# Kernel tuning notes

Measured on AMD Instinct MI355X. Metric: run time of the kernel, lower is better.

Reference implementation:

```python
import jax, jax.numpy as jnp
import numpy as np

N_STEPS = 5
STATE_DIM = 512
ANN_DIM = 256
N_NODES = 2048
N_EDGE_TYPES = 4


def setup_inputs() -> dict:
    key = jax.random.key(0)
    ks = jax.random.split(key, 12)
    D, E, N = STATE_DIM, N_EDGE_TYPES, N_NODES
    s = 0.02
    adjacency = (jax.random.uniform(ks[0], (N, N * 2 * E)) < 0.015).astype(jnp.float32)
    annotations = jax.random.normal(ks[1], (N, ANN_DIM), dtype=jnp.float32)
    W_prop = jax.random.normal(ks[2], (2 * E, D, D), dtype=jnp.float32) * s
    b_prop = jnp.zeros((2 * E, D), dtype=jnp.float32)
    Wz = jax.random.normal(ks[3], (D, D), dtype=jnp.float32) * s
    Uz = jax.random.normal(ks[4], (D, D), dtype=jnp.float32) * s
    bz = jnp.zeros((D,), dtype=jnp.float32)
    Wr = jax.random.normal(ks[5], (D, D), dtype=jnp.float32) * s
    Ur = jax.random.normal(ks[6], (D, D), dtype=jnp.float32) * s
    br = jnp.zeros((D,), dtype=jnp.float32)
    Wh = jax.random.normal(ks[7], (D, D), dtype=jnp.float32) * s
    Uh = jax.random.normal(ks[8], (D, D), dtype=jnp.float32) * s
    bh = jnp.zeros((D,), dtype=jnp.float32)
    return dict(adjacency=adjacency, annotations=annotations, W_prop=W_prop, b_prop=b_prop,
                Wz=Wz, Uz=Uz, bz=bz, Wr=Wr, Ur=Ur, br=br, Wh=Wh, Uh=Uh, bh=bh)


def reference(adjacency, annotations, W_prop, b_prop, Wz, Uz, bz, Wr, Ur, br, Wh, Uh, bh):
    N = annotations.shape[0]
    D = W_prop.shape[-1]
    # pad annotations into first columns of state (input1[:, :ann_dim] = annotations)
    h = jnp.zeros((N, D), dtype=annotations.dtype).at[:, :annotations.shape[1]].set(annotations)
    for _ in range(N_STEPS):
        # per-edge-type linear transforms: edge_type_list [2E, N, D]
        t = jnp.einsum('nd,edf->enf', h, W_prop) + b_prop[:, None, :]
        # adjacency aggregation: A is [N, N*2E] with per-edge-type column blocks
        a = adjacency @ t.reshape(-1, D)  # [N, D]
        # GRU node update (UpdateNet)
        z = jax.nn.sigmoid(a @ Wz + h @ Uz + bz)
        r = jax.nn.sigmoid(a @ Wr + h @ Ur + br)
        h_tilde = jnp.tanh(a @ Wh + (r * h) @ Uh + bh)
        h = (1.0 - z) * h + z * h_tilde
    return h
```

## Files before the change

kernel.cpp:

```cpp
#include <hip/hip_runtime.h>

typedef __attribute__((ext_vector_type(8))) short short8;
typedef __attribute__((ext_vector_type(4))) float floatx4;
typedef __attribute__((ext_vector_type(2))) unsigned uintx2;

#define NSTEPS 5
#define DD 512
#define ANN 256
#define NNODE 2048
#define NEDGE 8
#define NCOLS (NNODE * NEDGE)
#define MAXE 96
#define KP (NEDGE * DD)
#define NND (NNODE * DD)


typedef __attribute__((address_space(3))) unsigned lds_u32;
typedef const __attribute__((address_space(1))) unsigned g_u32;
__device__ __forceinline__ void gload16(const short* g, short* l) {
    __builtin_amdgcn_global_load_lds((g_u32*)g, (lds_u32*)l, 16, 0, 0);
}

__device__ inline float bf2f(unsigned short s) {
    unsigned u = ((unsigned)s) << 16;
    float f; __builtin_memcpy(&f, &u, 4);
    return f;
}
__device__ inline unsigned short f2bf(float f) {
    unsigned u; __builtin_memcpy(&u, &f, 4);
    u += 0x7fffu + ((u >> 16) & 1u);
    return (unsigned short)(u >> 16);
}
__device__ inline void split2(float x, unsigned short& hi, unsigned short& lo) {
    hi = f2bf(x);
    lo = f2bf(x - bf2f(hi));
}
__device__ inline void fo_write(short* __restrict__ Fhi, short* __restrict__ Flo,
                                int row, int col, float v) {
    unsigned short hs, ls;
    split2(v, hs, ls);
    size_t a = ((size_t)(row >> 4) * 64 + (col >> 3)) * 128 + ((row & 15) << 3) + (col & 7);
    Fhi[a] = (short)hs;
    Flo[a] = (short)ls;
}
__device__ inline void fo_write2(short* __restrict__ Fhi, short* __restrict__ Flo,
                                 int row, int c, float v0, float v1) {
    unsigned short h0, l0, h1, l1;
    split2(v0, h0, l0);
    split2(v1, h1, l1);
    size_t a = ((size_t)(row >> 4) * 64 + (c >> 3)) * 128 + ((row & 15) << 3) + (c & 7);
    *(unsigned*)(Fhi + a) = (unsigned)h0 | ((unsigned)h1 << 16);
    *(unsigned*)(Flo + a) = (unsigned)l0 | ((unsigned)l1 << 16);
}

__global__ __launch_bounds__(256) void k_init(const float* __restrict__ ann,
                                              float* __restrict__ h,
                                              short* __restrict__ HBhi,
                                              short* __restrict__ HBlo,
                                              int* __restrict__ cnt2,
                                              unsigned short* __restrict__ idx) {
    int n = blockIdx.x, t = threadIdx.x;
    int c = 2 * t;
    float v0 = 0.f, v1 = 0.f;
    if (c < ANN) {
        v0 = ann[(size_t)n * ANN + c];
        v1 = ann[(size_t)n * ANN + c + 1];
    }
    h[(size_t)n * DD + c]     = v0;
    h[(size_t)n * DD + c + 1] = v1;
    fo_write2(HBhi, HBlo, n, c, v0, v1);
    if (t < NEDGE) cnt2[n * NEDGE + t] = 0;
    unsigned* ip = (unsigned*)(idx + (size_t)n * NEDGE * MAXE);
    for (int j = t; j < NEDGE * MAXE / 2; j += 256)
        ip[j] = 2048u | (2048u << 16);
    if (n == 0) {
        h[(size_t)NNODE * DD + c]     = 0.f;
        h[(size_t)NNODE * DD + c + 1] = 0.f;
    }
}

__global__ __launch_bounds__(256) void k_build(const float* __restrict__ adj,
                                               int* __restrict__ cnt2,
                                               unsigned short* __restrict__ idx) {
    int n = blockIdx.x;
    const float* row = adj + (size_t)n * NCOLS;
    for (int j8 = threadIdx.x; j8 < NCOLS / 8; j8 += 256) {
        floatx4 a = *(const floatx4*)(row + j8 * 8);
        floatx4 b = *(const floatx4*)(row + j8 * 8 + 4);
        unsigned nz = 0;
        #pragma unroll
        for (int i = 0; i < 4; i++) {
            if (a[i] != 0.f) nz |= 1u << i;
            if (b[i] != 0.f) nz |= 1u << (4 + i);
        }
        while (nz) {
            int i = __builtin_ctz(nz);
            nz &= nz - 1;
            int j = j8 * 8 + i;
            int e = j >> 11;
            int m = j & (NNODE - 1);
            int p = atomicAdd(&cnt2[n * NEDGE + e], 1);
            if (p < MAXE) idx[((size_t)n * NEDGE + e) * MAXE + p] = (unsigned short)m;
        }
    }
}

__global__ __launch_bounds__(256) void k_transP(const float* __restrict__ W,
                                                short* __restrict__ Fhi,
                                                short* __restrict__ Flo, int K) {
    __shared__ float st[32][33];
    int tx = threadIdx.x & 31, ty = threadIdx.x >> 5;
    int k0 = blockIdx.x * 32, n0 = blockIdx.y * 32;
    #pragma unroll
    for (int i = 0; i < 4; i++)
        st[ty + i * 8][tx] = W[(size_t)(k0 + ty + i * 8) * DD + n0 + tx];
    __syncthreads();
    #pragma unroll
    for (int i = 0; i < 4; i++) {
        int n = n0 + ty + i * 8, k = k0 + tx;
        float v = st[tx][ty + i * 8];
        unsigned short hs, ls;
        split2(v, hs, ls);
        size_t a = ((size_t)(n >> 4) * (K >> 3) + (k >> 3)) * 128 + ((n & 15) << 3) + (k & 7);
        Fhi[a] = (short)hs;
        Flo[a] = (short)ls;
    }
}

__global__ __launch_bounds__(256) void k_transG(const float* __restrict__ s00,
                                                const float* __restrict__ s10,
                                                const float* __restrict__ s01,
                                                const float* __restrict__ s11,
                                                short* __restrict__ Fhi,
                                                short* __restrict__ Flo) {
    __shared__ float st[32][33];
    const int K = 2 * DD;
    int tx = threadIdx.x & 31, ty = threadIdx.x >> 5;
    int k0 = blockIdx.x * 32, n0 = blockIdx.y * 32;
    const float* sk0 = (n0 < DD) ? s00 : s01;
    const float* sk1 = (n0 < DD) ? s10 : s11;
    #pragma unroll
    for (int i = 0; i < 4; i++) {
        int k = k0 + ty + i * 8;
        const float* s = (k < DD) ? sk0 : sk1;
        st[ty + i * 8][tx] = s[(size_t)(k & (DD - 1)) * DD + ((n0 + tx) & (DD - 1))];
    }
    __syncthreads();
    #pragma unroll
    for (int i = 0; i < 4; i++) {
        int n = n0 + ty + i * 8, k = k0 + tx;
        float v = st[tx][ty + i * 8];
        unsigned short hs, ls;
        split2(v, hs, ls);
        size_t a = ((size_t)(n >> 4) * (K >> 3) + (k >> 3)) * 128 + ((n & 15) << 3) + (k & 7);
        Fhi[a] = (short)hs;
        Flo[a] = (short)ls;
    }
}

__global__ __launch_bounds__(256) void k_gather_all(const float* __restrict__ h,
                                                    const int* __restrict__ cnt2,
                                                    const unsigned short* __restrict__ idx,
                                                    short* __restrict__ Gbhi,
                                                    short* __restrict__ Gblo) {
    __shared__ unsigned short sidx[8 * MAXE];
    __shared__ int scnt[8];
    const int bid = blockIdx.x;
    const int ep = bid & 3;
    const int g  = bid >> 2;
    const int n0 = g * 4;
    const int t  = threadIdx.x;
    const int dn = t >> 6;
    const int th2 = t & 63;

    if (t < 8) scnt[t] = cnt2[(n0 + (t >> 1)) * NEDGE + 2 * ep + (t & 1)];
    {
        const unsigned* src0 = (const unsigned*)(idx + ((size_t)n0 * NEDGE + 2 * ep) * MAXE);
        for (int j = t; j < 384; j += 256) {
            int d = j / 96;
            int w = j - d * 96;
            ((unsigned*)sidx)[d * 96 + w] = src0[(size_t)d * (NEDGE * MAXE / 2) + w];
        }
    }
    __syncthreads();

    const float* hp = h + 8 * th2;

    floatx4 e0c0, e0c1, e1c0, e1c1;
    auto gather_edge = [&](int le, floatx4& o0, floatx4& o1) {
        int m = scnt[dn * 2 + le];
        m = m > MAXE ? MAXE : m;
        m = (m + 3) & ~3;
        const unsigned short* row = &sidx[dn * 192 + le * 96];
        floatx4 a0 = (floatx4){0.f, 0.f, 0.f, 0.f};
        floatx4 a1 = (floatx4){0.f, 0.f, 0.f, 0.f};
        floatx4 b0 = (floatx4){0.f, 0.f, 0.f, 0.f};
        floatx4 b1 = (floatx4){0.f, 0.f, 0.f, 0.f};
        for (int i = 0; i < m; i += 4) {
            uintx2 w = *(const uintx2*)(row + i);
            const float* r0 = hp + (size_t)(w[0] & 0xffffu) * DD;
            const float* r1 = hp + (size_t)(w[0] >> 16) * DD;
            const float* r2 = hp + (size_t)(w[1] & 0xffffu) * DD;
            const float* r3 = hp + (size_t)(w[1] >> 16) * DD;
            floatx4 v0 = *(const floatx4*)r0;
            floatx4 v1 = *(const floatx4*)(r0 + 4);
            floatx4 v2 = *(const floatx4*)r1;
            floatx4 v3 = *(const floatx4*)(r1 + 4);
            floatx4 v4 = *(const floatx4*)r2;
            floatx4 v5 = *(const floatx4*)(r2 + 4);
            floatx4 v6 = *(const floatx4*)r3;
            floatx4 v7 = *(const floatx4*)(r3 + 4);
            a0 += v0; a1 += v1; b0 += v2; b1 += v3;
            a0 += v4; a1 += v5; b0 += v6; b1 += v7;
        }
        o0 = a0 + b0;
        o1 = a1 + b1;
    };
    gather_edge(0, e0c0, e0c1);
    gather_edge(1, e1c0, e1c1);

    __syncthreads();

    #pragma unroll
    for (int le = 0; le < 2; le++) {
        floatx4 c0 = le ? e1c0 : e0c0;
        floatx4 c1 = le ? e1c1 : e0c1;
        int ge = 2 * ep + le;
        unsigned short hs[8], ls[8];
        #pragma unroll
        for (int j = 0; j < 4; j++) {
            split2(c0[j], hs[j], ls[j]);
            split2(c1[j], hs[4 + j], ls[4 + j]);
        }
        short8 hv, lv;
        #pragma unroll
        for (int j = 0; j < 8; j++) { hv[j] = (short)hs[j]; lv[j] = (short)ls[j]; }
        size_t a = ((size_t)(n0 >> 4) * 512 + ge * 64 + th2) * 128
                 + (size_t)((n0 & 15) + dn) * 8;
        *(short8*)(Gbhi + a) = hv;
        *(short8*)(Gblo + a) = lv;
    }
}

template<int MODE>
__global__ __launch_bounds__(256, 4) void k_gemm8(
    const short* __restrict__ A0hi, const short* __restrict__ A0lo,
    const short* __restrict__ A1hi, const short* __restrict__ A1lo,
    const short* __restrict__ Bhi,  const short* __restrict__ Blo,
    const float* __restrict__ bias0, const float* __restrict__ bias1,
    float* __restrict__ zbuf,
    float* __restrict__ h,
    short* __restrict__ Ohi, short* __restrict__ Olo,
    float* __restrict__ Pb) {

    __shared__ short S[24][512];

    const int tid = threadIdx.x;
    const int lane = tid & 63;
    const int wave = tid >> 6;
    const int wm = wave >> 1;
    const int wn = wave & 1;
    const int quad = lane >> 4;
    const int l16 = lane & 15;

    const int pbid = blockIdx.x;
    const int x = pbid & 7;
    const int j = pbid >> 3;
    const int mband = x * 4 + (j & 3);
    int kh, bx;
    if (MODE == 1) { kh = 0; bx = j >> 2; }
    else           { kh = (j >> 2) & 1; bx = j >> 3; }
    const int blockM = mband * 64;
    const int blockN = bx * 32;
    const int mt0 = blockM >> 4, nt0 = blockN >> 4;
    const int KCB = (MODE == 0) ? 512 : 128;
    const int bko = (MODE == 0) ? kh * 256 : (MODE == 2 ? kh * 64 : 0);
    const int Kloc = (MODE == 0) ? 2048 : (MODE == 1 ? 1024 : 512);

    const short* Ahi_s = (MODE == 2 && kh) ? A1hi : A0hi;
    const short* Alo_s = (MODE == 2 && kh) ? A1lo : A0lo;

    floatx4 acc[2];
    acc[0] = (floatx4){0.f, 0.f, 0.f, 0.f};
    acc[1] = (floatx4){0.f, 0.f, 0.f, 0.f};

    auto gaddr = [&](int k0, int s) -> const short* {
        if (s < 16) {
            int pl = s >> 3, u = s & 7;
            int mt = u >> 1, ks = u & 1;
            const short* base;
            int kc, stride;
            if (MODE == 0) {
                base = pl ? A0lo : A0hi;
                kc = kh * 256 + (k0 >> 3) + ks * 4;
                stride = 512;
            } else if (MODE == 1) {
                int seg = k0 >> 9;
                base = seg ? (pl ? A1lo : A1hi) : (pl ? A0lo : A0hi);
                kc = ((k0 & 511) >> 3) + ks * 4;
                stride = 64;
            } else {
                base = pl ? Alo_s : Ahi_s;
                kc = (k0 >> 3) + ks * 4;
                stride = 64;
            }
            return base + ((size_t)(mt0 + mt) * stride + kc) * 128;
        } else {
            int u = s - 16, pl = u >> 2, ks = (u >> 1) & 1, nt = u & 1;
            const short* base = pl ? Blo : Bhi;
            return base + ((size_t)(nt0 + nt) * KCB + bko + (k0 >> 3) + ks * 4) * 128;
        }
    };

    const short* gp[6];
    short* lp[6];
    #pragma unroll
    for (int jj = 0; jj < 6; jj++) {
        int s = jj * 4 + wave;
        gp[jj] = gaddr(0, s) + lane * 8;
        lp[jj] = &S[s][lane * 8];
    }

    const int SEGK = (MODE == 1) ? 512 : Kloc;
    #pragma unroll 1
    for (int seg = 0; seg < Kloc / SEGK; seg++) {
        if (MODE == 1 && seg == 1) {
            #pragma unroll
            for (int jj = 0; jj < 6; jj++) {
                int s = jj * 4 + wave;
                gp[jj] = gaddr(512, s) + lane * 8;
            }
        }
        #pragma unroll 1
        for (int k0 = 0; k0 < SEGK; k0 += 64) {
            #pragma unroll
            for (int jj = 0; jj < 6; jj++) {
                gload16(gp[jj], lp[jj]);
                gp[jj] += 1024;
            }
            __syncthreads();

            #pragma unroll
            for (int ks = 0; ks < 2; ks++) {
                short8 ah[2], al[2], bh, bl;
                #pragma unroll
                for (int mi = 0; mi < 2; mi++) {
                    ah[mi] = *(const short8*)&S[(wm * 2 + mi) * 2 + ks][lane * 8];
                    al[mi] = *(const short8*)&S[8 + (wm * 2 + mi) * 2 + ks][lane * 8];
                }
                bh = *(const short8*)&S[16 + ks * 2 + wn][lane * 8];
                bl = *(const short8*)&S[20 + ks * 2 + wn][lane * 8];
                #pragma unroll
                for (int mi = 0; mi < 2; mi++) {
                    acc[mi] = __builtin_amdgcn_mfma_f32_16x16x32_bf16(ah[mi], bh, acc[mi], 0, 0, 0);
                    acc[mi] = __builtin_amdgcn_mfma_f32_16x16x32_bf16(ah[mi], bl, acc[mi], 0, 0, 0);
                    acc[mi] = __builtin_amdgcn_mfma_f32_16x16x32_bf16(al[mi], bh, acc[mi], 0, 0, 0);
                }
            }
            __syncthreads();
        }
    }

    float* P = Pb + (size_t)kh * NND;
    #pragma unroll
    for (int mi = 0; mi < 2; mi++) {
        int gcol = blockN + wn * 16 + l16;
        #pragma unroll
        for (int r = 0; r < 4; r++) {
            int grow = blockM + wm * 32 + mi * 16 + quad * 4 + r;
            float v = acc[mi][r];
            if (MODE == 0 || MODE == 2) {
                P[(size_t)grow * DD + gcol] = v;
            } else {
                if (gcol < DD) {
                    size_t o = (size_t)grow * DD + gcol;
                    zbuf[o] = 1.f / (1.f + __expf(-(v + bias0[gcol])));
                } else {
                    int c = gcol - DD;
                    size_t o = (size_t)grow * DD + c;
                    float rr = 1.f / (1.f + __expf(-(v + bias1[c])));
                    fo_write(Ohi, Olo, grow, c, rr * h[o]);
                }
            }
        }
    }
}

__global__ __launch_bounds__(256) void k_combP(const float* __restrict__ Pb,
                                               const int* __restrict__ cnt2,
                                               const float* __restrict__ bp,
                                               short* __restrict__ Gahi,
                                               short* __restrict__ Galo) {
    int n = blockIdx.x, t = threadIdx.x;
    int c = 2 * t;
    float s0 = 0.f, s1 = 0.f;
    #pragma unroll
    for (int e = 0; e < NEDGE; e++) {
        float ce = (float)cnt2[n * NEDGE + e];
        s0 += ce * bp[e * DD + c];
        s1 += ce * bp[e * DD + c + 1];
    }
    size_t o = (size_t)n * DD + c;
    float v0 = Pb[o] + Pb[o + NND] + s0;
    float v1 = Pb[o + 1] + Pb[o + 1 + NND] + s1;
    fo_write2(Gahi, Galo, n, c, v0, v1);
}

__global__ __launch_bounds__(256) void k_combF(const float* __restrict__ Pb,
                                               const float* __restrict__ bh,
                                               const float* __restrict__ zbuf,
                                               float* __restrict__ h,
                                               short* __restrict__ HBhi,
                                               short* __restrict__ HBlo,
                                               float* __restrict__ outF) {
    int n = blockIdx.x, t = threadIdx.x;
    int c = 2 * t;
    size_t o = (size_t)n * DD + c;
    float hn0, hn1;
    {
        float v = Pb[o] + Pb[o + NND] + bh[c];
        hn0 = (1.f - zbuf[o]) * h[o] + zbuf[o] * tanhf(v);
    }
    {
        float v = Pb[o + 1] + Pb[o + 1 + NND] + bh[c + 1];
        hn1 = (1.f - zbuf[o + 1]) * h[o + 1] + zbuf[o + 1] * tanhf(v);
    }
    h[o] = hn0;
    h[o + 1] = hn1;
    fo_write2(HBhi, HBlo, n, c, hn0, hn1);
    outF[o] = hn0;
    outF[o + 1] = hn1;
}

extern "C" void kernel_launch(void* const* d_in, const int* in_sizes, int n_in,
                              void* d_out, int out_size, void* d_ws, size_t ws_size,
                              hipStream_t stream) {
    const float* adj = (const float*)d_in[0];
    const float* ann = (const float*)d_in[1];
    const float* Wp  = (const float*)d_in[2];
    const float* bp  = (const float*)d_in[3];
    const float* Wz  = (const float*)d_in[4];
    const float* Uz  = (const float*)d_in[5];
    const float* bz  = (const float*)d_in[6];
    const float* Wr  = (const float*)d_in[7];
    const float* Ur  = (const float*)d_in[8];
    const float* br  = (const float*)d_in[9];
    const float* Wh  = (const float*)d_in[10];
    const float* Uh  = (const float*)d_in[11];
    const float* bh  = (const float*)d_in[12];

    char* p = (char*)d_ws;
    float* h     = (float*)p; p += (size_t)(NNODE + 1) * DD * 4;
    float* abuf  = (float*)p; p += (size_t)NNODE * DD * 4;
    float* Pb    = (float*)p; p += (size_t)4 * NND * 4;
    short* Gbhi  = (short*)p; p += (size_t)NNODE * KP * 2;
    short* Gblo  = (short*)p; p += (size_t)NNODE * KP * 2;
    short* Gahi  = (short*)p; p += (size_t)NNODE * DD * 2;
    short* Galo  = (short*)p; p += (size_t)NNODE * DD * 2;
    short* HBhi  = (short*)p; p += (size_t)NNODE * DD * 2;
    short* HBlo  = (short*)p; p += (size_t)NNODE * DD * 2;
    short* RHhi  = (short*)p; p += (size_t)NNODE * DD * 2;
    short* RHlo  = (short*)p; p += (size_t)NNODE * DD * 2;
    short* WpThi = (short*)p; p += (size_t)DD * KP * 2;
    short* WpTlo = (short*)p; p += (size_t)DD * KP * 2;
    short* ZRhi  = (short*)p; p += (size_t)(2 * DD) * (2 * DD) * 2;
    short* ZRlo  = (short*)p; p += (size_t)(2 * DD) * (2 * DD) * 2;
    short* HThi  = (short*)p; p += (size_t)DD * (2 * DD) * 2;
    short* HTlo  = (short*)p; p += (size_t)DD * (2 * DD) * 2;
    unsigned short* idx = (unsigned short*)p;
    p += (size_t)NNODE * NEDGE * MAXE * 2;
    int* cnt2 = (int*)p; p += (size_t)NNODE * NEDGE * 4;

    float* outF = (float*)d_out;

    k_init<<<NNODE, 256, 0, stream>>>(ann, h, HBhi, HBlo, cnt2, idx);
    k_build<<<NNODE, 256, 0, stream>>>(adj, cnt2, idx);
    k_transP<<<dim3(KP / 32, DD / 32), 256, 0, stream>>>(Wp, WpThi, WpTlo, KP);
    k_transG<<<dim3(32, 32), 256, 0, stream>>>(Wz, Uz, Wr, Ur, ZRhi, ZRlo);
    k_transG<<<dim3(32, 16), 256, 0, stream>>>(Wh, Uh, Wh, Uh, HThi, HTlo);

    for (int s = 0; s < NSTEPS; s++) {
        k_gather_all<<<2048, 256, 0, stream>>>(h, cnt2, idx, Gbhi, Gblo);
        k_gemm8<0><<<1024, 256, 0, stream>>>(Gbhi, Gblo, nullptr, nullptr,
                                             WpThi, WpTlo, nullptr, nullptr,
                                             nullptr, nullptr, nullptr, nullptr, Pb);
        k_combP<<<NNODE, 256, 0, stream>>>(Pb, cnt2, bp, Gahi, Galo);
        k_gemm8<1><<<1024, 256, 0, stream>>>(Gahi, Galo, HBhi, HBlo,
                                             ZRhi, ZRlo, bz, br,
                                             abuf, h, RHhi, RHlo, nullptr);
        k_gemm8<2><<<1024, 256, 0, stream>>>(Gahi, Galo, RHhi, RHlo,
                                             HThi, HTlo, nullptr, nullptr,
                                             nullptr, nullptr, nullptr, nullptr, Pb);
        k_combF<<<NNODE, 256, 0, stream>>>(Pb, bh, abuf, h, HBhi, HBlo, outF);
    }
}
```

Before: 929.5 us.

## Double-buffer LDS tiles in k_gemm8 to overlap global loads with MFMA

Doubles the shared-memory staging buffer so the next K-tile is prefetched with global_load_lds while the MFMAs run on the current tile. One barrier per iteration is removed and the loop is flattened into a single K loop with recomputed addresses. The launch-bounds occupancy hint drops from 4 to 3 blocks per CU because the LDS footprint doubles. A risk is that the async LDS loads may not be waited on correctly before the single barrier.

```diff
diff --git a/kernel.cpp b/kernel.cpp
--- a/kernel.cpp
+++ b/kernel.cpp
@@ -243,7 +243,7 @@
 }
 
 template<int MODE>
-__global__ __launch_bounds__(256, 4) void k_gemm8(
+__global__ __launch_bounds__(256, 3) void k_gemm8(
     const short* __restrict__ A0hi, const short* __restrict__ A0lo,
     const short* __restrict__ A1hi, const short* __restrict__ A1lo,
     const short* __restrict__ Bhi,  const short* __restrict__ Blo,
@@ -253,7 +253,7 @@
     short* __restrict__ Ohi, short* __restrict__ Olo,
     float* __restrict__ Pb) {
 
-    __shared__ short S[24][512];
+    __shared__ short S[2][24][512];
 
     const int tid = threadIdx.x;
     const int lane = tid & 63;
@@ -312,53 +312,45 @@
         }
     };
 
-    const short* gp[6];
-    short* lp[6];
     #pragma unroll
     for (int jj = 0; jj < 6; jj++) {
         int s = jj * 4 + wave;
-        gp[jj] = gaddr(0, s) + lane * 8;
-        lp[jj] = &S[s][lane * 8];
-    }
-
-    const int SEGK = (MODE == 1) ? 512 : Kloc;
+        gload16(gaddr(0, s) + lane * 8, &S[0][s][lane * 8]);
+    }
+    __syncthreads();
+
+    const int NK = Kloc / 64;
+    int cur = 0;
     #pragma unroll 1
-    for (int seg = 0; seg < Kloc / SEGK; seg++) {
-        if (MODE == 1 && seg == 1) {
+    for (int ki = 0; ki < NK; ki++) {
+        if (ki + 1 < NK) {
+            int kn = (ki + 1) * 64;
             #pragma unroll
             for (int jj = 0; jj < 6; jj++) {
                 int s = jj * 4 + wave;
-                gp[jj] = gaddr(512, s) + lane * 8;
+                gload16(gaddr(kn, s) + lane * 8, &S[cur ^ 1][s][lane * 8]);
             }
         }
-        #pragma unroll 1
-        for (int k0 = 0; k0 < SEGK; k0 += 64) {
+
+        #pragma unroll
+        for (int ks = 0; ks < 2; ks++) {
+            short8 ah[2], al[2], bh, bl;
             #pragma unroll
-            for (int jj = 0; jj < 6; jj++) {
-                gload16(gp[jj], lp[jj]);
-                gp[jj] += 1024;
+            for (int mi = 0; mi < 2; mi++) {
+                ah[mi] = *(const short8*)&S[cur][(wm * 2 + mi) * 2 + ks][lane * 8];
+                al[mi] = *(const short8*)&S[cur][8 + (wm * 2 + mi) * 2 + ks][lane * 8];
             }
-            __syncthreads();
-
+            bh = *(const short8*)&S[cur][16 + ks * 2 + wn][lane * 8];
+            bl = *(const short8*)&S[cur][20 + ks * 2 + wn][lane * 8];
             #pragma unroll
-            for (int ks = 0; ks < 2; ks++) {
-                short8 ah[2], al[2], bh, bl;
-                #pragma unroll
-                for (int mi = 0; mi < 2; mi++) {
-                    ah[mi] = *(const short8*)&S[(wm * 2 + mi) * 2 + ks][lane * 8];
-                    al[mi] = *(const short8*)&S[8 + (wm * 2 + mi) * 2 + ks][lane * 8];
-                }
-                bh = *(const short8*)&S[16 + ks * 2 + wn][lane * 8];
-                bl = *(const short8*)&S[20 + ks * 2 + wn][lane * 8];
-                #pragma unroll
-                for (int mi = 0; mi < 2; mi++) {
-                    acc[mi] = __builtin_amdgcn_mfma_f32_16x16x32_bf16(ah[mi], bh, acc[mi], 0, 0, 0);
-                    acc[mi] = __builtin_amdgcn_mfma_f32_16x16x32_bf16(ah[mi], bl, acc[mi], 0, 0, 0);
-                    acc[mi] = __builtin_amdgcn_mfma_f32_16x16x32_bf16(al[mi], bh, acc[mi], 0, 0, 0);
-                }
+            for (int mi = 0; mi < 2; mi++) {
+                acc[mi] = __builtin_amdgcn_mfma_f32_16x16x32_bf16(ah[mi], bh, acc[mi], 0, 0, 0);
+                acc[mi] = __builtin_amdgcn_mfma_f32_16x16x32_bf16(ah[mi], bl, acc[mi], 0, 0, 0);
+                acc[mi] = __builtin_amdgcn_mfma_f32_16x16x32_bf16(al[mi], bh, acc[mi], 0, 0, 0);
             }
-            __syncthreads();
-        }
+        }
+        __syncthreads();
+        cur ^= 1;
     }
 
     float* P = Pb + (size_t)kh * NND;
```

Result: slower. 1.329 ms (+42.9%).
